# Optimization experiments

Measured on AMD Instinct MI355X. Metric: run time of the kernel, lower is better.

The kernel has to match this reference:

```python
import jax, jax.numpy as jnp
import numpy as np

N, D, R, E = 10000, 1024, 8, 80000


def setup_inputs() -> dict:
    key = jax.random.key(0)
    ks = jax.random.split(key, 8)
    s = 1.0 / np.sqrt(D)
    x = jax.random.normal(ks[0], (N, D), dtype=jnp.float32)
    edge_index = jax.random.randint(ks[1], (2, E), 0, N, dtype=jnp.int64)
    edge_type = jax.random.randint(ks[2], (E,), 0, R, dtype=jnp.int64)
    weight = jax.random.normal(ks[3], (R, D, D), dtype=jnp.float32) * s  # per-relation W_r
    root = jax.random.normal(ks[4], (D, D), dtype=jnp.float32) * s      # root/self-loop weight
    bias = jnp.zeros((D,), dtype=jnp.float32)
    w_gate = jax.random.normal(ks[5], (2 * D, D), dtype=jnp.float32) * (1.0 / np.sqrt(2 * D))
    b_gate = jnp.zeros((D,), dtype=jnp.float32)
    return {"x": x, "edge_index": edge_index, "edge_type": edge_type,
            "weight": weight, "root": root, "bias": bias,
            "w_gate": w_gate, "b_gate": b_gate}


def _rgcn(x, edge_index, edge_type, weight, root, bias):
    # PyG RGCNConv (aggr='mean'): per relation r, mean-aggregate x[src] into dst,
    # then transform by W_r (aggregate-then-transform, equivalent by linearity).
    src, dst = edge_index[0], edge_index[1]
    msgs = x[src]                                   # [E, D] gather
    out = x @ root + bias                           # root/self connection
    n = x.shape[0]
    for r in range(weight.shape[0]):                # small fixed relation loop
        mask = (edge_type == r).astype(x.dtype)     # [E]
        sums = jax.ops.segment_sum(msgs * mask[:, None], dst, num_segments=n)
        cnt = jax.ops.segment_sum(mask, dst, num_segments=n)
        mean = sums / jnp.maximum(cnt, 1.0)[:, None]
        out = out + mean @ weight[r]
    return out


def reference(x, edge_index, edge_type, weight, root, bias, w_gate, b_gate):
    u = _rgcn(x, edge_index, edge_type, weight, root, bias)
    # dropout p=0 -> identity
    z = jnp.concatenate([u, x], axis=1) @ w_gate + b_gate
    h = jnp.tanh(u) * z + x * (1.0 - z)
    return h
```

## Files before the change

kernel.cpp:

```cpp
#include <hip/hip_runtime.h>
#include <math.h>

typedef unsigned short u16;
typedef __attribute__((ext_vector_type(8))) short bf16x8;
typedef __attribute__((ext_vector_type(4))) float f32x4;

static constexpr int kN = 10000;
static constexpr int kNpad = 10240;
static constexpr int kD = 1024;
static constexpr int kR = 8;
static constexpr int kE = 80000;
static constexpr int kKz = 2 * kD;
static constexpr int kCrows = kNpad * (kR + 1);
static constexpr int kTilesY = kCrows / 256;

#define GLB(p) ((const __attribute__((address_space(1))) unsigned int*)(const void*)(p))
#define LDSP(p) ((__attribute__((address_space(3))) unsigned int*)(p))

__device__ __forceinline__ u16 f2bf(float f) {
    union { float f; unsigned int i; } c; c.f = f;
    unsigned int u = c.i;
    return (u16)((u + 0x7FFFu + ((u >> 16) & 1u)) >> 16);
}
__device__ __forceinline__ float bf2f(u16 u) {
    union { unsigned int i; float f; } c; c.i = ((unsigned int)u) << 16;
    return c.f;
}
__device__ __forceinline__ ushort4 f2bf4(float4 v) {
    ushort4 o; o.x = f2bf(v.x); o.y = f2bf(v.y); o.z = f2bf(v.z); o.w = f2bf(v.w);
    return o;
}

__global__ void zero16(uint4* __restrict__ p, long n16) {
    long i = (long)blockIdx.x * blockDim.x + threadIdx.x;
    long st = (long)gridDim.x * blockDim.x;
    uint4 z = make_uint4(0, 0, 0, 0);
    for (; i < n16; i += st) p[i] = z;
}

__global__ void mark_edges(const int* __restrict__ src, const int* __restrict__ dst,
                           const int* __restrict__ etype,
                           int* __restrict__ cntd, int* __restrict__ flag) {
    int e = blockIdx.x * blockDim.x + threadIdx.x;
    if (e < kE) {
        atomicAdd(&cntd[dst[e]], 1);
        flag[etype[e] * kN + src[e]] = 1;
    }
}

__global__ __launch_bounds__(1024) void scan_rowptr(const int* __restrict__ cnt,
                                                    int* __restrict__ rowptr,
                                                    int* __restrict__ cursor) {
    __shared__ int wsum[16];
    __shared__ int carry;
    const int tid = threadIdx.x;
    const int lane = tid & 63;
    const int w = tid >> 6;
    if (tid == 0) carry = 0;
    const int nchunk = (kN + 1024) / 1024;
    for (int ch = 0; ch < nchunk; ++ch) {
        int idx = ch * 1024 + tid;
        int v = (idx < kN) ? cnt[idx] : 0;
        int s = v;
#pragma unroll
        for (int off = 1; off < 64; off <<= 1) {
            int t = __shfl_up(s, off, 64);
            if (lane >= off) s += t;
        }
        if (lane == 63) wsum[w] = s;
        __syncthreads();
        if (w == 0 && lane < 16) {
            int t = wsum[lane];
#pragma unroll
            for (int off = 1; off < 16; off <<= 1) {
                int tt = __shfl_up(t, off, 64);
                if (lane >= off) t += tt;
            }
            wsum[lane] = t;
        }
        __syncthreads();
        int wpre = (w > 0) ? wsum[w - 1] : 0;
        int incl = s + wpre + carry;
        int excl = incl - v;
        if (idx <= kN) rowptr[idx] = excl;
        if (idx < kN) cursor[idx] = 0;
        __syncthreads();
        if (tid == 1023) carry = incl;
        __syncthreads();
    }
}

__global__ __launch_bounds__(1024) void compact_scan(const int* __restrict__ flag,
                                                     int* __restrict__ row_src,
                                                     int* __restrict__ pos_tab,
                                                     int* __restrict__ relcnt9) {
    const int tid = threadIdx.x;
    if (blockIdx.x == kR) {
        for (int i = tid; i < kNpad; i += 1024) row_src[i] = i;
        if (tid == 0) relcnt9[0] = kN;
        return;
    }
    const int r = blockIdx.x;
    const int base = kNpad * (r + 1);
    __shared__ int wsum[16];
    __shared__ int carry;
    const int lane = tid & 63;
    const int w = tid >> 6;
    if (tid == 0) carry = 0;
    const int nchunk = (kN + 1023) / 1024;
    for (int ch = 0; ch < nchunk; ++ch) {
        int idx = ch * 1024 + tid;
        int v = (idx < kN) ? flag[r * kN + idx] : 0;
        int s = v;
#pragma unroll
        for (int off = 1; off < 64; off <<= 1) {
            int t = __shfl_up(s, off, 64);
            if (lane >= off) s += t;
        }
        if (lane == 63) wsum[w] = s;
        __syncthreads();
        if (w == 0 && lane < 16) {
            int t = wsum[lane];
#pragma unroll
            for (int off = 1; off < 16; off <<= 1) {
                int tt = __shfl_up(t, off, 64);
                if (lane >= off) t += tt;
            }
            wsum[lane] = t;
        }
        __syncthreads();
        int wpre = (w > 0) ? wsum[w - 1] : 0;
        int incl = s + wpre + carry;
        int excl = incl - v;
        if (idx < kN && v) {
            row_src[base + excl] = idx;
            pos_tab[r * kN + idx] = base + excl;
        }
        __syncthreads();
        if (tid == 1023) carry = incl;
        __syncthreads();
    }
    if (tid == 0) relcnt9[r + 1] = carry;
}

__global__ void fill_edges(const int* __restrict__ src, const int* __restrict__ dst,
                           const int* __restrict__ etype, const int* __restrict__ rowptr,
                           int* __restrict__ cursor, const int* __restrict__ pos_tab,
                           int* __restrict__ erec) {
    int e = blockIdx.x * blockDim.x + threadIdx.x;
    if (e < kE) {
        int d = dst[e], r = etype[e], s = src[e];
        int pos = rowptr[d] + atomicAdd(&cursor[d], 1);
        erec[pos] = (pos_tab[r * kN + s] << 3) | r;
    }
}

__global__ void cvt_x(const float* __restrict__ x, u16* __restrict__ ga) {
    int row = blockIdx.x;
    int c = threadIdx.x << 2;
    float4 v = *reinterpret_cast<const float4*>(x + (size_t)row * kD + c);
    *reinterpret_cast<ushort4*>(ga + (size_t)row * kKz + kD + c) = f2bf4(v);
}

__global__ void transpose_to_bf16(const float* __restrict__ S, u16* __restrict__ D,
                                  int rows, int cols, int ldD) {
    S += (size_t)blockIdx.z * rows * cols;
    D += (size_t)blockIdx.z * rows * cols;
    __shared__ float t[32][33];
    int c0 = blockIdx.x * 32, r0 = blockIdx.y * 32;
    int x = threadIdx.x, y = threadIdx.y;
#pragma unroll
    for (int i = 0; i < 32; i += 8)
        t[y + i][x] = S[(size_t)(r0 + y + i) * cols + c0 + x];
    __syncthreads();
#pragma unroll
    for (int i = 0; i < 32; i += 8)
        D[(size_t)(c0 + y + i) * ldD + r0 + x] = f2bf(t[x][y + i]);
}

__global__ __launch_bounds__(256) void aggregate(const u16* __restrict__ yc,
                                                 const float* __restrict__ bias,
                                                 const int* __restrict__ rowptr,
                                                 const int* __restrict__ erec,
                                                 u16* __restrict__ ga) {
    const int d = blockIdx.x;
    const int c = threadIdx.x << 2;
    const int e0 = rowptr[d], e1 = rowptr[d + 1];

    __shared__ float rs[kR];
    if (threadIdx.x == 0) {
        int cc[kR] = {0, 0, 0, 0, 0, 0, 0, 0};
        for (int e = e0; e < e1; ++e) cc[erec[e] & 7]++;
#pragma unroll
        for (int r = 0; r < kR; ++r) rs[r] = 1.0f / fmaxf((float)cc[r], 1.0f);
    }
    __syncthreads();

    ushort4 rv = *reinterpret_cast<const ushort4*>(yc + (size_t)d * kD + c);
    float4 bv = *reinterpret_cast<const float4*>(bias + c);
    float4 acc = make_float4(bf2f(rv.x) + bv.x, bf2f(rv.y) + bv.y,
                             bf2f(rv.z) + bv.z, bf2f(rv.w) + bv.w);

    for (int e = e0; e < e1; ++e) {
        int rec = erec[e];
        int rel = rec & 7;
        int pos = rec >> 3;
        float sc = rs[rel];
        ushort4 v = *reinterpret_cast<const ushort4*>(yc + (size_t)pos * kD + c);
        acc.x += sc * bf2f(v.x); acc.y += sc * bf2f(v.y);
        acc.z += sc * bf2f(v.z); acc.w += sc * bf2f(v.w);
    }
    *reinterpret_cast<ushort4*>(ga + (size_t)d * kKz + c) = f2bf4(acc);
}

__global__ __launch_bounds__(256, 2) void gemm_compact(
    const u16* __restrict__ xb, int ldx,
    const u16* __restrict__ Bt9,
    const int* __restrict__ row_src, const int* __restrict__ relcnt9,
    u16* __restrict__ yc)
{
    const int t = blockIdx.y;
    const int relidx = t / 40;
    const int lt = t - relidx * 40;
    if (lt * 256 >= relcnt9[relidx]) return;

    __shared__ u16 sA[256 * 32];
    __shared__ u16 sB[128 * 32];

    const int tid = threadIdx.x;
    const int wave = tid >> 6;
    const int lane = tid & 63;

    const int row0 = t * 256;
    const int col0 = blockIdx.x * 128;

    const int srow4 = lane >> 2;
    const int scol = (lane & 3) * 8;

    const u16* gA[4];
    u16* lA[4];
#pragma unroll
    for (int q = 0; q < 4; ++q) {
        int r = wave * 64 + q * 16;
        int srcrow = row_src[row0 + r + srow4];
        gA[q] = xb + (size_t)srcrow * ldx + scol;
        lA[q] = sA + r * 32;
    }
    const u16* gB[2];
    u16* lB[2];
#pragma unroll
    for (int p = 0; p < 2; ++p) {
        int r = p * 64 + wave * 16;
        gB[p] = Bt9 + (size_t)(relidx * kD + col0 + r + srow4) * kD + scol;
        lB[p] = sB + r * 32;
    }

    const int mq = (wave >> 1) * 128;
    const int nq = (wave & 1) * 64;
    const int fm = lane & 15;
    const int fk = (lane >> 4) * 8;

    f32x4 zf = {0.0f, 0.0f, 0.0f, 0.0f};
    f32x4 acc[8][4];
#pragma unroll
    for (int i = 0; i < 8; ++i)
#pragma unroll
        for (int j = 0; j < 4; ++j) acc[i][j] = zf;

    for (int k0 = 0; k0 < kD; k0 += 32) {
        __syncthreads();
#pragma unroll
        for (int q = 0; q < 4; ++q)
            __builtin_amdgcn_global_load_lds(GLB(gA[q]), LDSP(lA[q]), 16, 0, 0);
#pragma unroll
        for (int p = 0; p < 2; ++p)
            __builtin_amdgcn_global_load_lds(GLB(gB[p]), LDSP(lB[p]), 16, 0, 0);
#pragma unroll
        for (int q = 0; q < 4; ++q) gA[q] += 32;
#pragma unroll
        for (int p = 0; p < 2; ++p) gB[p] += 32;
        __syncthreads();

        bf16x8 af[8], bfr[4];
#pragma unroll
        for (int i = 0; i < 8; ++i)
            af[i] = *reinterpret_cast<const bf16x8*>(&sA[(mq + i * 16 + fm) * 32 + fk]);
#pragma unroll
        for (int j = 0; j < 4; ++j)
            bfr[j] = *reinterpret_cast<const bf16x8*>(&sB[(nq + j * 16 + fm) * 32 + fk]);
#pragma unroll
        for (int i = 0; i < 8; ++i)
#pragma unroll
            for (int j = 0; j < 4; ++j)
                acc[i][j] = __builtin_amdgcn_mfma_f32_16x16x32_bf16(bfr[j], af[i], acc[i][j], 0, 0, 0);
    }

    const int cq = (lane >> 4) * 4;
#pragma unroll
    for (int i = 0; i < 8; ++i) {
        int row = row0 + mq + i * 16 + fm;
#pragma unroll
        for (int j = 0; j < 4; ++j) {
            int col = col0 + nq + j * 16 + cq;
            f32x4 v = acc[i][j];
            ushort4 o;
            o.x = f2bf(v[0]); o.y = f2bf(v[1]); o.z = f2bf(v[2]); o.w = f2bf(v[3]);
            *reinterpret_cast<ushort4*>(yc + (size_t)row * kD + col) = o;
        }
    }
}

__global__ __launch_bounds__(256) void gemm_mfma_gate(
    const u16* __restrict__ A, int lda,
    const u16* __restrict__ Bt, int ldb, int K,
    int M, const float* __restrict__ bias,
    float* __restrict__ Cf, const u16* __restrict__ uga, const float* __restrict__ xo)
{
    __shared__ u16 sA[128 * 32];
    __shared__ u16 sB[128 * 32];

    const int tid = threadIdx.x;
    const int wave = tid >> 6;
    const int lane = tid & 63;

    const int row0 = blockIdx.y * 128;
    const int col0 = blockIdx.x * 128;

    const int srow = wave * 16 + (lane >> 2);
    const int scol = (lane & 3) * 8;

    const u16* gA0 = A + (size_t)(row0 + srow) * lda + scol;
    const u16* gA1 = A + (size_t)(row0 + 64 + srow) * lda + scol;
    const u16* gB0 = Bt + (size_t)(col0 + srow) * ldb + scol;
    const u16* gB1 = Bt + (size_t)(col0 + 64 + srow) * ldb + scol;

    u16* lA0 = sA + (wave * 16) * 32;
    u16* lA1 = sA + (64 + wave * 16) * 32;
    u16* lB0 = sB + (wave * 16) * 32;
    u16* lB1 = sB + (64 + wave * 16) * 32;

    const int mq = (wave >> 1) * 64;
    const int nq = (wave & 1) * 64;
    const int fm = lane & 15;
    const int fk = (lane >> 4) * 8;

    f32x4 zf = {0.0f, 0.0f, 0.0f, 0.0f};
    f32x4 acc[4][4];
#pragma unroll
    for (int i = 0; i < 4; ++i)
#pragma unroll
        for (int j = 0; j < 4; ++j) acc[i][j] = zf;

    for (int k0 = 0; k0 < K; k0 += 32) {
        __syncthreads();
        __builtin_amdgcn_global_load_lds(GLB(gA0), LDSP(lA0), 16, 0, 0);
        __builtin_amdgcn_global_load_lds(GLB(gA1), LDSP(lA1), 16, 0, 0);
        __builtin_amdgcn_global_load_lds(GLB(gB0), LDSP(lB0), 16, 0, 0);
        __builtin_amdgcn_global_load_lds(GLB(gB1), LDSP(lB1), 16, 0, 0);
        gA0 += 32; gA1 += 32; gB0 += 32; gB1 += 32;
        __syncthreads();

        bf16x8 af[4], bfr[4];
#pragma unroll
        for (int i = 0; i < 4; ++i)
            af[i] = *reinterpret_cast<const bf16x8*>(&sA[(mq + i * 16 + fm) * 32 + fk]);
#pragma unroll
        for (int j = 0; j < 4; ++j)
            bfr[j] = *reinterpret_cast<const bf16x8*>(&sB[(nq + j * 16 + fm) * 32 + fk]);
#pragma unroll
        for (int i = 0; i < 4; ++i)
#pragma unroll
            for (int j = 0; j < 4; ++j)
                acc[i][j] = __builtin_amdgcn_mfma_f32_16x16x32_bf16(bfr[j], af[i], acc[i][j], 0, 0, 0);
    }

    const int cq = (lane >> 4) * 4;
#pragma unroll
    for (int i = 0; i < 4; ++i) {
        int row = row0 + mq + i * 16 + fm;
        if (row >= M) continue;
#pragma unroll
        for (int j = 0; j < 4; ++j) {
            int col = col0 + nq + j * 16 + cq;
            f32x4 v = acc[i][j];
            float4 bv = *reinterpret_cast<const float4*>(bias + col);
            v[0] += bv.x; v[1] += bv.y; v[2] += bv.z; v[3] += bv.w;
            ushort4 ur = *reinterpret_cast<const ushort4*>(uga + (size_t)row * kKz + col);
            float4 xr = *reinterpret_cast<const float4*>(xo + (size_t)row * kD + col);
            float4 h;
            h.x = tanhf(bf2f(ur.x)) * v[0] + xr.x * (1.0f - v[0]);
            h.y = tanhf(bf2f(ur.y)) * v[1] + xr.y * (1.0f - v[1]);
            h.z = tanhf(bf2f(ur.z)) * v[2] + xr.z * (1.0f - v[2]);
            h.w = tanhf(bf2f(ur.w)) * v[3] + xr.w * (1.0f - v[3]);
            *reinterpret_cast<float4*>(Cf + (size_t)row * kD + col) = h;
        }
    }
}

extern "C" void kernel_launch(void* const* d_in, const int* in_sizes, int n_in,
                              void* d_out, int out_size, void* d_ws, size_t ws_size,
                              hipStream_t stream) {
    (void)in_sizes; (void)n_in; (void)out_size; (void)ws_size;

    const float* x     = (const float*)d_in[0];
    const int* eidx    = (const int*)d_in[1];
    const int* etype   = (const int*)d_in[2];
    const float* weight= (const float*)d_in[3];
    const float* root  = (const float*)d_in[4];
    const float* bias  = (const float*)d_in[5];
    const float* wgate = (const float*)d_in[6];
    const float* bgate = (const float*)d_in[7];
    float* out = (float*)d_out;

    const int* src = eidx;
    const int* dst = eidx + kE;

    char* ws = (char*)d_ws;
    size_t off = 0;
    u16* yc   = (u16*)(ws + off);    off += (size_t)kCrows * kD * 2;
    u16* ga   = (u16*)(ws + off);    off += (size_t)kNpad * kKz * 2;
    u16* Bt9  = (u16*)(ws + off);    off += (size_t)(kR + 1) * kD * kD * 2;
    u16* wg_t = (u16*)(ws + off);    off += (size_t)kD * kKz * 2;
    int* cntd    = (int*)(ws + off); off += (size_t)kN * 4;
    int* flag    = (int*)(ws + off); off += (size_t)kR * kN * 4;
    int* row_src = (int*)(ws + off); off += (size_t)kCrows * 4;
    int* pos_tab = (int*)(ws + off); off += (size_t)kR * kN * 4;
    int* rowp    = (int*)(ws + off); off += (size_t)(kN + 16) * 4;
    int* curs    = (int*)(ws + off); off += (size_t)kN * 4;
    int* erec    = (int*)(ws + off); off += (size_t)kE * 4;
    int* relcnt9 = (int*)(ws + off); off += 16 * 4;

    zero16<<<180, 256, 0, stream>>>((uint4*)cntd, (long)(kN + kR * kN + kCrows) / 4);

    mark_edges<<<(kE + 255) / 256, 256, 0, stream>>>(src, dst, etype, cntd, flag);
    scan_rowptr<<<1, 1024, 0, stream>>>(cntd, rowp, curs);
    compact_scan<<<kR + 1, 1024, 0, stream>>>(flag, row_src, pos_tab, relcnt9);
    fill_edges<<<(kE + 255) / 256, 256, 0, stream>>>(src, dst, etype, rowp, curs,
                                                     pos_tab, erec);

    zero16<<<256, 256, 0, stream>>>((uint4*)(ga + (size_t)kN * kKz),
                                    (long)(kNpad - kN) * kKz * 2 / 16);

    cvt_x<<<kN, 256, 0, stream>>>(x, ga);

    {
        dim3 b(32, 8);
        transpose_to_bf16<<<dim3(kD / 32, kD / 32, 1), b, 0, stream>>>(root, Bt9, kD, kD, kD);
        transpose_to_bf16<<<dim3(kD / 32, kD / 32, kR), b, 0, stream>>>(
            weight, Bt9 + (size_t)kD * kD, kD, kD, kD);
        transpose_to_bf16<<<dim3(kD / 32, kKz / 32, 1), b, 0, stream>>>(wgate, wg_t, kKz, kD, kKz);
    }

    dim3 g1(kD / 128, kTilesY);
    gemm_compact<<<g1, 256, 0, stream>>>(ga + kD, kKz, Bt9, row_src, relcnt9, yc);

    aggregate<<<kN, 256, 0, stream>>>(yc, bias, rowp, erec, ga);

    dim3 g2(kD / 128, kNpad / 128);
    gemm_mfma_gate<<<g2, 256, 0, stream>>>(ga, kKz, wg_t, kKz, kKz, kN, bgate, out, ga, x);
}
```

Measured before the change: 496.6 us.

## Use 32x32x16 MFMA in compact GEMM and merge small setup kernels

The compact relation GEMM switches from 16x16x32 to 32x32x16 bf16 MFMA tiles, with a 4x2 grid of 16-float accumulators per wave and matching fragment loads and epilogue stores. The aim is fewer LDS fragment reads per MFMA and higher matrix-core throughput. Separately, the rowptr scan is folded into the compaction kernel as an extra block, and zeroing of the padded ga rows is folded into cvt_x, removing two kernel launches. The new epilogue writes scattered 8-byte chunks, which may hurt store coalescing.

```diff
diff --git a/kernel.cpp b/kernel.cpp
--- a/kernel.cpp
+++ b/kernel.cpp
@@ -4,6 +4,7 @@
 typedef unsigned short u16;
 typedef __attribute__((ext_vector_type(8))) short bf16x8;
 typedef __attribute__((ext_vector_type(4))) float f32x4;
+typedef __attribute__((ext_vector_type(16))) float f32x16;
 
 static constexpr int kN = 10000;
 static constexpr int kNpad = 10240;
@@ -48,65 +49,62 @@
     }
 }
 
-__global__ __launch_bounds__(1024) void scan_rowptr(const int* __restrict__ cnt,
-                                                    int* __restrict__ rowptr,
-                                                    int* __restrict__ cursor) {
-    __shared__ int wsum[16];
-    __shared__ int carry;
-    const int tid = threadIdx.x;
-    const int lane = tid & 63;
-    const int w = tid >> 6;
-    if (tid == 0) carry = 0;
-    const int nchunk = (kN + 1024) / 1024;
-    for (int ch = 0; ch < nchunk; ++ch) {
-        int idx = ch * 1024 + tid;
-        int v = (idx < kN) ? cnt[idx] : 0;
-        int s = v;
-#pragma unroll
-        for (int off = 1; off < 64; off <<= 1) {
-            int t = __shfl_up(s, off, 64);
-            if (lane >= off) s += t;
-        }
-        if (lane == 63) wsum[w] = s;
-        __syncthreads();
-        if (w == 0 && lane < 16) {
-            int t = wsum[lane];
-#pragma unroll
-            for (int off = 1; off < 16; off <<= 1) {
-                int tt = __shfl_up(t, off, 64);
-                if (lane >= off) t += tt;
-            }
-            wsum[lane] = t;
-        }
-        __syncthreads();
-        int wpre = (w > 0) ? wsum[w - 1] : 0;
-        int incl = s + wpre + carry;
-        int excl = incl - v;
-        if (idx <= kN) rowptr[idx] = excl;
-        if (idx < kN) cursor[idx] = 0;
-        __syncthreads();
-        if (tid == 1023) carry = incl;
-        __syncthreads();
-    }
-}
-
-__global__ __launch_bounds__(1024) void compact_scan(const int* __restrict__ flag,
-                                                     int* __restrict__ row_src,
-                                                     int* __restrict__ pos_tab,
-                                                     int* __restrict__ relcnt9) {
+__global__ __launch_bounds__(1024) void build_meta(const int* __restrict__ flag,
+                                                   const int* __restrict__ cntd,
+                                                   int* __restrict__ row_src,
+                                                   int* __restrict__ pos_tab,
+                                                   int* __restrict__ relcnt9,
+                                                   int* __restrict__ rowptr,
+                                                   int* __restrict__ cursor) {
     const int tid = threadIdx.x;
     if (blockIdx.x == kR) {
         for (int i = tid; i < kNpad; i += 1024) row_src[i] = i;
         if (tid == 0) relcnt9[0] = kN;
         return;
     }
+    const int lane = tid & 63;
+    const int w = tid >> 6;
+    __shared__ int wsum[16];
+    __shared__ int carry;
+    if (tid == 0) carry = 0;
+
+    if (blockIdx.x == kR + 1) {
+        const int nchunk = (kN + 1024) / 1024;
+        for (int ch = 0; ch < nchunk; ++ch) {
+            int idx = ch * 1024 + tid;
+            int v = (idx < kN) ? cntd[idx] : 0;
+            int s = v;
+#pragma unroll
+            for (int off = 1; off < 64; off <<= 1) {
+                int t = __shfl_up(s, off, 64);
+                if (lane >= off) s += t;
+            }
+            if (lane == 63) wsum[w] = s;
+            __syncthreads();
+            if (w == 0 && lane < 16) {
+                int t = wsum[lane];
+#pragma unroll
+                for (int off = 1; off < 16; off <<= 1) {
+                    int tt = __shfl_up(t, off, 64);
+                    if (lane >= off) t += tt;
+                }
+                wsum[lane] = t;
+            }
+            __syncthreads();
+            int wpre = (w > 0) ? wsum[w - 1] : 0;
+            int incl = s + wpre + carry;
+            int excl = incl - v;
+            if (idx <= kN) rowptr[idx] = excl;
+            if (idx < kN) cursor[idx] = 0;
+            __syncthreads();
+            if (tid == 1023) carry = incl;
+            __syncthreads();
+        }
+        return;
+    }
+
     const int r = blockIdx.x;
     const int base = kNpad * (r + 1);
-    __shared__ int wsum[16];
-    __shared__ int carry;
-    const int lane = tid & 63;
-    const int w = tid >> 6;
-    if (tid == 0) carry = 0;
     const int nchunk = (kN + 1023) / 1024;
     for (int ch = 0; ch < nchunk; ++ch) {
         int idx = ch * 1024 + tid;
@@ -158,8 +156,14 @@
 __global__ void cvt_x(const float* __restrict__ x, u16* __restrict__ ga) {
     int row = blockIdx.x;
     int c = threadIdx.x << 2;
-    float4 v = *reinterpret_cast<const float4*>(x + (size_t)row * kD + c);
-    *reinterpret_cast<ushort4*>(ga + (size_t)row * kKz + kD + c) = f2bf4(v);
+    if (row < kN) {
+        float4 v = *reinterpret_cast<const float4*>(x + (size_t)row * kD + c);
+        *reinterpret_cast<ushort4*>(ga + (size_t)row * kKz + kD + c) = f2bf4(v);
+    } else {
+        ushort4 z = {0, 0, 0, 0};
+        *reinterpret_cast<ushort4*>(ga + (size_t)row * kKz + c) = z;
+        *reinterpret_cast<ushort4*>(ga + (size_t)row * kKz + kD + c) = z;
+    }
 }
 
 __global__ void transpose_to_bf16(const float* __restrict__ S, u16* __restrict__ D,
@@ -257,15 +261,16 @@
 
     const int mq = (wave >> 1) * 128;
     const int nq = (wave & 1) * 64;
-    const int fm = lane & 15;
-    const int fk = (lane >> 4) * 8;
-
-    f32x4 zf = {0.0f, 0.0f, 0.0f, 0.0f};
-    f32x4 acc[8][4];
-#pragma unroll
-    for (int i = 0; i < 8; ++i)
-#pragma unroll
-        for (int j = 0; j < 4; ++j) acc[i][j] = zf;
+    const int fm = lane & 31;
+    const int fk = (lane >> 5) * 8;
+
+    f32x16 acc[4][2];
+#pragma unroll
+    for (int i = 0; i < 4; ++i)
+#pragma unroll
+        for (int j = 0; j < 2; ++j)
+#pragma unroll
+            for (int r = 0; r < 16; ++r) acc[i][j][r] = 0.0f;
 
     for (int k0 = 0; k0 < kD; k0 += 32) {
         __syncthreads();
@@ -281,31 +286,45 @@
         for (int p = 0; p < 2; ++p) gB[p] += 32;
         __syncthreads();
 
-        bf16x8 af[8], bfr[4];
-#pragma unroll
-        for (int i = 0; i < 8; ++i)
-            af[i] = *reinterpret_cast<const bf16x8*>(&sA[(mq + i * 16 + fm) * 32 + fk]);
-#pragma unroll
-        for (int j = 0; j < 4; ++j)
-            bfr[j] = *reinterpret_cast<const bf16x8*>(&sB[(nq + j * 16 + fm) * 32 + fk]);
-#pragma unroll
-        for (int i = 0; i < 8; ++i)
-#pragma unroll
-            for (int j = 0; j < 4; ++j)
-                acc[i][j] = __builtin_amdgcn_mfma_f32_16x16x32_bf16(bfr[j], af[i], acc[i][j], 0, 0, 0);
-    }
-
-    const int cq = (lane >> 4) * 4;
-#pragma unroll
-    for (int i = 0; i < 8; ++i) {
-        int row = row0 + mq + i * 16 + fm;
-#pragma unroll
-        for (int j = 0; j < 4; ++j) {
-            int col = col0 + nq + j * 16 + cq;
-            f32x4 v = acc[i][j];
-            ushort4 o;
-            o.x = f2bf(v[0]); o.y = f2bf(v[1]); o.z = f2bf(v[2]); o.w = f2bf(v[3]);
-            *reinterpret_cast<ushort4*>(yc + (size_t)row * kD + col) = o;
+        bf16x8 af[4][2], bfr[2][2];
+#pragma unroll
+        for (int s = 0; s < 2; ++s) {
+#pragma unroll
+            for (int i = 0; i < 4; ++i)
+                af[i][s] = *reinterpret_cast<const bf16x8*>(
+                    &sA[(mq + i * 32 + fm) * 32 + s * 16 + fk]);
+#pragma unroll
+            for (int j = 0; j < 2; ++j)
+                bfr[j][s] = *reinterpret_cast<const bf16x8*>(
+                    &sB[(nq + j * 32 + fm) * 32 + s * 16 + fk]);
+        }
+#pragma unroll
+        for (int s = 0; s < 2; ++s)
+#pragma unroll
+            for (int i = 0; i < 4; ++i)
+#pragma unroll
+                for (int j = 0; j < 2; ++j)
+                    acc[i][j] = __builtin_amdgcn_mfma_f32_32x32x16_bf16(
+                        bfr[j][s], af[i][s], acc[i][j], 0, 0, 0);
+    }
+
+    const int half4 = (lane >> 5) * 4;
+#pragma unroll
+    for (int i = 0; i < 4; ++i) {
+        int row = row0 + mq + i * 32 + fm;
+#pragma unroll
+        for (int j = 0; j < 2; ++j) {
+            int colb = col0 + nq + j * 32 + half4;
+#pragma unroll
+            for (int g = 0; g < 4; ++g) {
+                int col = colb + 8 * g;
+                ushort4 o;
+                o.x = f2bf(acc[i][j][4 * g + 0]);
+                o.y = f2bf(acc[i][j][4 * g + 1]);
+                o.z = f2bf(acc[i][j][4 * g + 2]);
+                o.w = f2bf(acc[i][j][4 * g + 3]);
+                *reinterpret_cast<ushort4*>(yc + (size_t)row * kD + col) = o;
+            }
         }
     }
 }
@@ -433,15 +452,12 @@
     zero16<<<180, 256, 0, stream>>>((uint4*)cntd, (long)(kN + kR * kN + kCrows) / 4);
 
     mark_edges<<<(kE + 255) / 256, 256, 0, stream>>>(src, dst, etype, cntd, flag);
-    scan_rowptr<<<1, 1024, 0, stream>>>(cntd, rowp, curs);
-    compact_scan<<<kR + 1, 1024, 0, stream>>>(flag, row_src, pos_tab, relcnt9);
+    build_meta<<<kR + 2, 1024, 0, stream>>>(flag, cntd, row_src, pos_tab, relcnt9,
+                                            rowp, curs);
     fill_edges<<<(kE + 255) / 256, 256, 0, stream>>>(src, dst, etype, rowp, curs,
                                                      pos_tab, erec);
 
-    zero16<<<256, 256, 0, stream>>>((uint4*)(ga + (size_t)kN * kKz),
-                                    (long)(kNpad - kN) * kKz * 2 / 16);
-
-    cvt_x<<<kN, 256, 0, stream>>>(x, ga);
+    cvt_x<<<kNpad, 256, 0, stream>>>(x, ga);
 
     {
         dim3 b(32, 8);
```

After: 511.2 us. +2.9%, slower.

## Merge metadata kernels, widen aggregate loads, and use nontemporal stores

Applied to the files above, without the earlier changes.

Merges the rowptr scan and the per-relation compaction into one launch, and folds the zeroing of the padded rows into cvt_x, which cuts two kernel launches. The aggregate kernel now uses 128 threads, each loading 8 bf16 values with 16-byte nontemporal loads, and counts relations in parallel across 8 threads instead of one. The GEMM epilogues write through nontemporal stores with packed bf16 pairs. Nontemporal hints may hurt reuse of yc, which aggregate reads back shortly after it is written.

```diff
diff --git a/kernel.cpp b/kernel.cpp
--- a/kernel.cpp
+++ b/kernel.cpp
@@ -4,6 +4,8 @@
 typedef unsigned short u16;
 typedef __attribute__((ext_vector_type(8))) short bf16x8;
 typedef __attribute__((ext_vector_type(4))) float f32x4;
+typedef __attribute__((ext_vector_type(4))) unsigned int u32x4;
+typedef __attribute__((ext_vector_type(2))) unsigned int u32x2;
 
 static constexpr int kN = 10000;
 static constexpr int kNpad = 10240;
@@ -26,6 +28,12 @@
     union { unsigned int i; float f; } c; c.i = ((unsigned int)u) << 16;
     return c.f;
 }
+__device__ __forceinline__ float bflo(unsigned int w) {
+    union { unsigned int i; float f; } c; c.i = w << 16; return c.f;
+}
+__device__ __forceinline__ float bfhi(unsigned int w) {
+    union { unsigned int i; float f; } c; c.i = w & 0xFFFF0000u; return c.f;
+}
 __device__ __forceinline__ ushort4 f2bf4(float4 v) {
     ushort4 o; o.x = f2bf(v.x); o.y = f2bf(v.y); o.z = f2bf(v.z); o.w = f2bf(v.w);
     return o;
@@ -48,65 +56,62 @@
     }
 }
 
-__global__ __launch_bounds__(1024) void scan_rowptr(const int* __restrict__ cnt,
-                                                    int* __restrict__ rowptr,
-                                                    int* __restrict__ cursor) {
-    __shared__ int wsum[16];
-    __shared__ int carry;
-    const int tid = threadIdx.x;
-    const int lane = tid & 63;
-    const int w = tid >> 6;
-    if (tid == 0) carry = 0;
-    const int nchunk = (kN + 1024) / 1024;
-    for (int ch = 0; ch < nchunk; ++ch) {
-        int idx = ch * 1024 + tid;
-        int v = (idx < kN) ? cnt[idx] : 0;
-        int s = v;
-#pragma unroll
-        for (int off = 1; off < 64; off <<= 1) {
-            int t = __shfl_up(s, off, 64);
-            if (lane >= off) s += t;
-        }
-        if (lane == 63) wsum[w] = s;
-        __syncthreads();
-        if (w == 0 && lane < 16) {
-            int t = wsum[lane];
-#pragma unroll
-            for (int off = 1; off < 16; off <<= 1) {
-                int tt = __shfl_up(t, off, 64);
-                if (lane >= off) t += tt;
-            }
-            wsum[lane] = t;
-        }
-        __syncthreads();
-        int wpre = (w > 0) ? wsum[w - 1] : 0;
-        int incl = s + wpre + carry;
-        int excl = incl - v;
-        if (idx <= kN) rowptr[idx] = excl;
-        if (idx < kN) cursor[idx] = 0;
-        __syncthreads();
-        if (tid == 1023) carry = incl;
-        __syncthreads();
-    }
-}
-
-__global__ __launch_bounds__(1024) void compact_scan(const int* __restrict__ flag,
-                                                     int* __restrict__ row_src,
-                                                     int* __restrict__ pos_tab,
-                                                     int* __restrict__ relcnt9) {
+__global__ __launch_bounds__(1024) void build_meta(const int* __restrict__ flag,
+                                                   const int* __restrict__ cntd,
+                                                   int* __restrict__ row_src,
+                                                   int* __restrict__ pos_tab,
+                                                   int* __restrict__ relcnt9,
+                                                   int* __restrict__ rowptr,
+                                                   int* __restrict__ cursor) {
     const int tid = threadIdx.x;
     if (blockIdx.x == kR) {
         for (int i = tid; i < kNpad; i += 1024) row_src[i] = i;
         if (tid == 0) relcnt9[0] = kN;
         return;
     }
+    const int lane = tid & 63;
+    const int w = tid >> 6;
+    __shared__ int wsum[16];
+    __shared__ int carry;
+    if (tid == 0) carry = 0;
+
+    if (blockIdx.x == kR + 1) {
+        const int nchunk = (kN + 1024) / 1024;
+        for (int ch = 0; ch < nchunk; ++ch) {
+            int idx = ch * 1024 + tid;
+            int v = (idx < kN) ? cntd[idx] : 0;
+            int s = v;
+#pragma unroll
+            for (int off = 1; off < 64; off <<= 1) {
+                int t = __shfl_up(s, off, 64);
+                if (lane >= off) s += t;
+            }
+            if (lane == 63) wsum[w] = s;
+            __syncthreads();
+            if (w == 0 && lane < 16) {
+                int t = wsum[lane];
+#pragma unroll
+                for (int off = 1; off < 16; off <<= 1) {
+                    int tt = __shfl_up(t, off, 64);
+                    if (lane >= off) t += tt;
+                }
+                wsum[lane] = t;
+            }
+            __syncthreads();
+            int wpre = (w > 0) ? wsum[w - 1] : 0;
+            int incl = s + wpre + carry;
+            int excl = incl - v;
+            if (idx <= kN) rowptr[idx] = excl;
+            if (idx < kN) cursor[idx] = 0;
+            __syncthreads();
+            if (tid == 1023) carry = incl;
+            __syncthreads();
+        }
+        return;
+    }
+
     const int r = blockIdx.x;
     const int base = kNpad * (r + 1);
-    __shared__ int wsum[16];
-    __shared__ int carry;
-    const int lane = tid & 63;
-    const int w = tid >> 6;
-    if (tid == 0) carry = 0;
     const int nchunk = (kN + 1023) / 1024;
     for (int ch = 0; ch < nchunk; ++ch) {
         int idx = ch * 1024 + tid;
@@ -158,8 +163,14 @@
 __global__ void cvt_x(const float* __restrict__ x, u16* __restrict__ ga) {
     int row = blockIdx.x;
     int c = threadIdx.x << 2;
-    float4 v = *reinterpret_cast<const float4*>(x + (size_t)row * kD + c);
-    *reinterpret_cast<ushort4*>(ga + (size_t)row * kKz + kD + c) = f2bf4(v);
+    if (row < kN) {
+        float4 v = *reinterpret_cast<const float4*>(x + (size_t)row * kD + c);
+        *reinterpret_cast<ushort4*>(ga + (size_t)row * kKz + kD + c) = f2bf4(v);
+    } else {
+        ushort4 z = {0, 0, 0, 0};
+        *reinterpret_cast<ushort4*>(ga + (size_t)row * kKz + c) = z;
+        *reinterpret_cast<ushort4*>(ga + (size_t)row * kKz + kD + c) = z;
+    }
 }
 
 __global__ void transpose_to_bf16(const float* __restrict__ S, u16* __restrict__ D,
@@ -178,39 +189,53 @@
         D[(size_t)(c0 + y + i) * ldD + r0 + x] = f2bf(t[x][y + i]);
 }
 
-__global__ __launch_bounds__(256) void aggregate(const u16* __restrict__ yc,
+__global__ __launch_bounds__(128) void aggregate(const u16* __restrict__ yc,
                                                  const float* __restrict__ bias,
                                                  const int* __restrict__ rowptr,
                                                  const int* __restrict__ erec,
                                                  u16* __restrict__ ga) {
     const int d = blockIdx.x;
-    const int c = threadIdx.x << 2;
+    const int c = threadIdx.x << 3;
     const int e0 = rowptr[d], e1 = rowptr[d + 1];
 
     __shared__ float rs[kR];
-    if (threadIdx.x == 0) {
-        int cc[kR] = {0, 0, 0, 0, 0, 0, 0, 0};
-        for (int e = e0; e < e1; ++e) cc[erec[e] & 7]++;
-#pragma unroll
-        for (int r = 0; r < kR; ++r) rs[r] = 1.0f / fmaxf((float)cc[r], 1.0f);
+    if (threadIdx.x < kR) {
+        int cc = 0;
+        for (int e = e0; e < e1; ++e) cc += ((erec[e] & 7) == (int)threadIdx.x);
+        rs[threadIdx.x] = 1.0f / fmaxf((float)cc, 1.0f);
     }
     __syncthreads();
 
-    ushort4 rv = *reinterpret_cast<const ushort4*>(yc + (size_t)d * kD + c);
-    float4 bv = *reinterpret_cast<const float4*>(bias + c);
-    float4 acc = make_float4(bf2f(rv.x) + bv.x, bf2f(rv.y) + bv.y,
-                             bf2f(rv.z) + bv.z, bf2f(rv.w) + bv.w);
+    float acc[8];
+    {
+        u32x4 rv = __builtin_nontemporal_load(
+            reinterpret_cast<const u32x4*>(yc + (size_t)d * kD + c));
+        float4 b0 = *reinterpret_cast<const float4*>(bias + c);
+        float4 b1 = *reinterpret_cast<const float4*>(bias + c + 4);
+        acc[0] = bflo(rv.x) + b0.x; acc[1] = bfhi(rv.x) + b0.y;
+        acc[2] = bflo(rv.y) + b0.z; acc[3] = bfhi(rv.y) + b0.w;
+        acc[4] = bflo(rv.z) + b1.x; acc[5] = bfhi(rv.z) + b1.y;
+        acc[6] = bflo(rv.w) + b1.z; acc[7] = bfhi(rv.w) + b1.w;
+    }
 
     for (int e = e0; e < e1; ++e) {
         int rec = erec[e];
-        int rel = rec & 7;
+        float sc = rs[rec & 7];
         int pos = rec >> 3;
-        float sc = rs[rel];
-        ushort4 v = *reinterpret_cast<const ushort4*>(yc + (size_t)pos * kD + c);
-        acc.x += sc * bf2f(v.x); acc.y += sc * bf2f(v.y);
-        acc.z += sc * bf2f(v.z); acc.w += sc * bf2f(v.w);
-    }
-    *reinterpret_cast<ushort4*>(ga + (size_t)d * kKz + c) = f2bf4(acc);
+        u32x4 v = __builtin_nontemporal_load(
+            reinterpret_cast<const u32x4*>(yc + (size_t)pos * kD + c));
+        acc[0] += sc * bflo(v.x); acc[1] += sc * bfhi(v.x);
+        acc[2] += sc * bflo(v.y); acc[3] += sc * bfhi(v.y);
+        acc[4] += sc * bflo(v.z); acc[5] += sc * bfhi(v.z);
+        acc[6] += sc * bflo(v.w); acc[7] += sc * bfhi(v.w);
+    }
+
+    u32x4 o;
+    o.x = (unsigned int)f2bf(acc[0]) | ((unsigned int)f2bf(acc[1]) << 16);
+    o.y = (unsigned int)f2bf(acc[2]) | ((unsigned int)f2bf(acc[3]) << 16);
+    o.z = (unsigned int)f2bf(acc[4]) | ((unsigned int)f2bf(acc[5]) << 16);
+    o.w = (unsigned int)f2bf(acc[6]) | ((unsigned int)f2bf(acc[7]) << 16);
+    *reinterpret_cast<u32x4*>(ga + (size_t)d * kKz + c) = o;
 }
 
 __global__ __launch_bounds__(256, 2) void gemm_compact(
@@ -303,9 +328,11 @@
         for (int j = 0; j < 4; ++j) {
             int col = col0 + nq + j * 16 + cq;
             f32x4 v = acc[i][j];
-            ushort4 o;
-            o.x = f2bf(v[0]); o.y = f2bf(v[1]); o.z = f2bf(v[2]); o.w = f2bf(v[3]);
-            *reinterpret_cast<ushort4*>(yc + (size_t)row * kD + col) = o;
+            u32x2 o;
+            o.x = (unsigned int)f2bf(v[0]) | ((unsigned int)f2bf(v[1]) << 16);
+            o.y = (unsigned int)f2bf(v[2]) | ((unsigned int)f2bf(v[3]) << 16);
+            __builtin_nontemporal_store(
+                o, reinterpret_cast<u32x2*>(yc + (size_t)row * kD + col));
         }
     }
 }
@@ -387,12 +414,13 @@
             v[0] += bv.x; v[1] += bv.y; v[2] += bv.z; v[3] += bv.w;
             ushort4 ur = *reinterpret_cast<const ushort4*>(uga + (size_t)row * kKz + col);
             float4 xr = *reinterpret_cast<const float4*>(xo + (size_t)row * kD + col);
-            float4 h;
-            h.x = tanhf(bf2f(ur.x)) * v[0] + xr.x * (1.0f - v[0]);
-            h.y = tanhf(bf2f(ur.y)) * v[1] + xr.y * (1.0f - v[1]);
-            h.z = tanhf(bf2f(ur.z)) * v[2] + xr.z * (1.0f - v[2]);
-            h.w = tanhf(bf2f(ur.w)) * v[3] + xr.w * (1.0f - v[3]);
-            *reinterpret_cast<float4*>(Cf + (size_t)row * kD + col) = h;
+            f32x4 h;
+            h[0] = tanhf(bf2f(ur.x)) * v[0] + xr.x * (1.0f - v[0]);
+            h[1] = tanhf(bf2f(ur.y)) * v[1] + xr.y * (1.0f - v[1]);
+            h[2] = tanhf(bf2f(ur.z)) * v[2] + xr.z * (1.0f - v[2]);
+            h[3] = tanhf(bf2f(ur.w)) * v[3] + xr.w * (1.0f - v[3]);
+            __builtin_nontemporal_store(
+                h, reinterpret_cast<f32x4*>(Cf + (size_t)row * kD + col));
         }
     }
 }
@@ -433,15 +461,12 @@
     zero16<<<180, 256, 0, stream>>>((uint4*)cntd, (long)(kN + kR * kN + kCrows) / 4);
 
     mark_edges<<<(kE + 255) / 256, 256, 0, stream>>>(src, dst, etype, cntd, flag);
-    scan_rowptr<<<1, 1024, 0, stream>>>(cntd, rowp, curs);
-    compact_scan<<<kR + 1, 1024, 0, stream>>>(flag, row_src, pos_tab, relcnt9);
+    build_meta<<<kR + 2, 1024, 0, stream>>>(flag, cntd, row_src, pos_tab, relcnt9,
+                                            rowp, curs);
     fill_edges<<<(kE + 255) / 256, 256, 0, stream>>>(src, dst, etype, rowp, curs,
                                                      pos_tab, erec);
 
-    zero16<<<256, 256, 0, stream>>>((uint4*)(ga + (size_t)kN * kKz),
-                                    (long)(kNpad - kN) * kKz * 2 / 16);
-
-    cvt_x<<<kN, 256, 0, stream>>>(x, ga);
+    cvt_x<<<kNpad, 256, 0, stream>>>(x, ga);
 
     {
         dim3 b(32, 8);
@@ -454,7 +479,7 @@
     dim3 g1(kD / 128, kTilesY);
     gemm_compact<<<g1, 256, 0, stream>>>(ga + kD, kKz, Bt9, row_src, relcnt9, yc);
 
-    aggregate<<<kN, 256, 0, stream>>>(yc, bias, rowp, erec, ga);
+    aggregate<<<kN, 128, 0, stream>>>(yc, bias, rowp, erec, ga);
 
     dim3 g2(kD / 128, kNpad / 128);
     gemm_mfma_gate<<<g2, 256, 0, stream>>>(ga, kKz, wg_t, kKz, kKz, kN, bgate, out, ga, x);
```

After: 558.7 us. 1.13x slower.
